# Kernel tuning notes

Hardware: AMD Instinct MI355X
Metric: run time of the kernel (lower is better)

Reference implementation:

```python
import jax, jax.numpy as jnp
import numpy as np

UNITS = 1024
EMBED = 512
K = 32000
HIDDEN_LAYERS = 2
BATCH = 64
SEQ = 256
ALPHA = 0.2  # leaky_relu slope


def _leaky_relu(z):
    return jnp.where(z > 0, z, ALPHA * z)


def setup_inputs() -> dict:
    key = jax.random.key(0)
    ks = jax.random.split(key, 10)
    s_in = 1.0 / np.sqrt(UNITS)
    s_e = 1.0 / np.sqrt(EMBED)
    return {
        "x": jax.random.randint(ks[0], (BATCH, SEQ), 0, K),
        "x_embedding": jax.random.normal(ks[1], (K, EMBED), dtype=jnp.float32) * 0.05,
        "w_y": jax.random.normal(ks[2], (UNITS, UNITS), dtype=jnp.float32) * s_in,
        "w_x": jax.random.normal(ks[3], (EMBED, UNITS), dtype=jnp.float32) * s_e,
        "b_in": jax.random.uniform(ks[4], (UNITS,), dtype=jnp.float32, minval=-0.05, maxval=0.05),
        "w_hidden": jax.random.normal(ks[5], (HIDDEN_LAYERS, UNITS, UNITS), dtype=jnp.float32) * s_in,
        "b_hidden": jax.random.uniform(ks[6], (HIDDEN_LAYERS, UNITS), dtype=jnp.float32, minval=-0.05, maxval=0.05),
        "w_out": jax.random.normal(ks[7], (UNITS, UNITS), dtype=jnp.float32) * s_in,
        "b_out": jax.random.uniform(ks[8], (UNITS,), dtype=jnp.float32, minval=-0.05, maxval=0.05),
        "h0": jax.random.uniform(ks[9], (1, UNITS), dtype=jnp.float32, minval=-0.05, maxval=0.05),
    }


def reference(x, x_embedding, w_y, w_x, b_in, w_hidden, b_hidden, w_out, b_out, h0):
    n = x.shape[0]
    # Gather all embeddings up front: [n, T, E] -> time-major [T, n, E]
    xe_all = jnp.swapaxes(x_embedding[x], 0, 1)

    def step(y0, xe):
        # MLPUnit: sum of input projections + bias, inner activation
        h = _leaky_relu(y0 @ w_y + xe @ w_x + b_in)

        def layer(hc, wb):
            w, bb = wb
            return _leaky_relu(hc @ w + bb), None

        h, _ = jax.lax.scan(layer, h, (w_hidden, b_hidden))
        y1 = y0 + (h @ w_out + b_out)  # highway residual
        return y1, y1

    y0 = jnp.broadcast_to(h0, (n, h0.shape[1]))
    _, yr = jax.lax.scan(step, y0, xe_all)  # [T, n, units]
    return jnp.swapaxes(yr, 0, 1)  # [n, T, units]
```

## Files before the change

### kernel.cpp

```cpp
#include <hip/hip_runtime.h>


constexpr int B = 64, T = 256, U = 1024, E = 512;
constexpr int BU = B * U;
constexpr int APITCH = 1156;
constexpr int RPITCH = 264;
constexpr int WOPITCH = 9;

#define LRELU(v) ((v) > 0.f ? (v) : 0.2f * (v))

using f4 = float __attribute__((ext_vector_type(4)));

__device__ __forceinline__ void llc_store(float* p, float v) {
  __hip_atomic_store(p, v, __ATOMIC_RELAXED, __HIP_MEMORY_SCOPE_AGENT);
}
__device__ __forceinline__ unsigned llc_flag(const unsigned* p) {
  return __hip_atomic_load(p, __ATOMIC_RELAXED, __HIP_MEMORY_SCOPE_AGENT);
}
__device__ __forceinline__ void llc_post(unsigned* p, unsigned v) {
  __hip_atomic_store(p, v, __ATOMIC_RELAXED, __HIP_MEMORY_SCOPE_AGENT);
}

#define COMPUTE_ACC(WB)                                          \
  do {                                                           \
    _Pragma("unroll") for (int r = 0; r < 8; ++r) acc[r] =       \
        (f4){0.f, 0.f, 0.f, 0.f};                                \
    _Pragma("unroll") for (int q = 0; q < 4; ++q) {              \
      const f4 w0 = WB[4 * q], w1 = WB[4 * q + 1];               \
      const f4 w2 = WB[4 * q + 2], w3 = WB[4 * q + 3];           \
      const int ab = abase_k + 4 * q;                            \
      _Pragma("unroll") for (int r = 0; r < 8; ++r) {            \
        f4 a = *(const f4*)&a_s[r * APITCH + ab];                \
        acc[r] += a.x * w0 + a.y * w1 + a.z * w2 + a.w * w3;     \
      }                                                          \
    }                                                            \
  } while (0)

__global__ void k_init(unsigned* __restrict__ flags) {
  int tid = blockIdx.x * 256 + threadIdx.x;
  if (tid < 512) flags[tid] = 0u;
}

__global__ __launch_bounds__(256) void k_xproj(
    const int* __restrict__ x, const float* __restrict__ emb,
    const float* __restrict__ w_x, const float* __restrict__ b_in,
    float* __restrict__ xp) {
  __shared__ float a_s[64][36];
  __shared__ float w_s[32][64];
  __shared__ int idxs[64];
  const int tid = threadIdx.x;
  const int m0 = blockIdx.x * 64;
  const int c0 = blockIdx.y * 64;
  if (tid < 64) {
    int m = m0 + tid;
    idxs[tid] = x[(m & 63) * T + (m >> 6)];
  }
  __syncthreads();
  const int rq = tid >> 4, cq = tid & 15;
  float acc[4][4] = {};
  for (int k0 = 0; k0 < E; k0 += 32) {
#pragma unroll
    for (int rep = 0; rep < 8; ++rep) {
      int e = rep * 256 + tid;
      int r = e >> 5, k = e & 31;
      a_s[r][k] = emb[(size_t)idxs[r] * E + k0 + k];
    }
#pragma unroll
    for (int rep = 0; rep < 2; ++rep) {
      int e = rep * 256 + tid;
      int kr = e >> 4, q = e & 15;
      *(float4*)&w_s[kr][4 * q] =
          *(const float4*)(w_x + (size_t)(k0 + kr) * U + c0 + 4 * q);
    }
    __syncthreads();
#pragma unroll
    for (int kc = 0; kc < 32; kc += 4) {
      float4 a4[4], w4[4];
#pragma unroll
      for (int i = 0; i < 4; ++i) a4[i] = *(const float4*)&a_s[4 * rq + i][kc];
#pragma unroll
      for (int kk = 0; kk < 4; ++kk)
        w4[kk] = *(const float4*)&w_s[kc + kk][4 * cq];
#pragma unroll
      for (int i = 0; i < 4; ++i) {
        const float av[4] = {a4[i].x, a4[i].y, a4[i].z, a4[i].w};
#pragma unroll
        for (int kk = 0; kk < 4; ++kk) {
          acc[i][0] += av[kk] * w4[kk].x;
          acc[i][1] += av[kk] * w4[kk].y;
          acc[i][2] += av[kk] * w4[kk].z;
          acc[i][3] += av[kk] * w4[kk].w;
        }
      }
    }
    __syncthreads();
  }
  const float4 bb = *(const float4*)(b_in + c0 + 4 * cq);
  const float bv[4] = {bb.x, bb.y, bb.z, bb.w};
#pragma unroll
  for (int i = 0; i < 4; ++i) {
    float4 o;
    o.x = acc[i][0] + bv[0];
    o.y = acc[i][1] + bv[1];
    o.z = acc[i][2] + bv[2];
    o.w = acc[i][3] + bv[3];
    *(float4*)(xp + (size_t)(m0 + 4 * rq + i) * U + c0 + 4 * cq) = o;
  }
}

__global__ __launch_bounds__(512, 2) void k_seq(
    const float* __restrict__ xp, const float* __restrict__ w_y,
    const float* __restrict__ w_h, const float* __restrict__ b_h,
    const float* __restrict__ w_out, const float* __restrict__ b_out,
    const float* __restrict__ h0, float* __restrict__ out,
    float* __restrict__ slots, unsigned* __restrict__ flags) {
  __shared__ float a_s[8 * APITCH];
  __shared__ float red2[64 * RPITCH];
  __shared__ float c2_s[32], u0_s[32];
  const int tid = threadIdx.x;
  const int bid = blockIdx.x;
  const int cg = ((bid & 7) << 2) | ((bid >> 3) & 3);
  const int rg = bid >> 5;
  const int w = tid >> 6, l = tid & 63;
  const int ci = l & 7;
  const int sp = w * 8 + (l >> 3);
  const int cb = 4 * ci, k0 = 16 * sp;
  const int abase_k = 36 * (sp >> 1) + 16 * (sp & 1);
  const int frow = 8 * rg + (tid >> 5);
  const int fu = 32 * cg + (tid & 31);
  const int tb = tid >> 8;
  const int kq = ((tid & 255) + 8 * cg) & 255;
  const int lofs = 36 * (kq >> 3) + ((4 * kq) & 31);

  float* const wos = red2;
  float* const wys = a_s;
  f4 w2reg[16];
#pragma unroll
  for (int jj = 0; jj < 16; ++jj) w2reg[jj] = (f4){0.f, 0.f, 0.f, 0.f};
  f4 c2a = (f4){0.f, 0.f, 0.f, 0.f}, u0a = (f4){0.f, 0.f, 0.f, 0.f};
  {
    f4 nx0, nx1, nx2, nx3, nwy;
    {
      const float* wo = w_out + (size_t)tid * U;
      nx0 = *(const f4*)wo;
      nx1 = *(const f4*)(wo + 4);
      const float* wo2 = w_out + (size_t)(tid + 512) * U;
      nx2 = *(const f4*)wo2;
      nx3 = *(const f4*)(wo2 + 4);
      if (tid < 64)
        nwy = *(const f4*)(w_y + (size_t)(tid >> 3) * U + 32 * cg +
                           4 * (tid & 7));
    }
    for (int mi = 0; mi < 128; ++mi) {
      const int m0 = mi * 8;
#pragma unroll
      for (int q = 0; q < 4; ++q) {
        wos[tid * WOPITCH + q] = nx0[q];
        wos[tid * WOPITCH + 4 + q] = nx1[q];
        wos[(tid + 512) * WOPITCH + q] = nx2[q];
        wos[(tid + 512) * WOPITCH + 4 + q] = nx3[q];
      }
      if (tid < 64) *(f4*)&wys[(tid >> 3) * 36 + 4 * (tid & 7)] = nwy;
      __syncthreads();
      if (mi < 127) {
        const int m1 = m0 + 8;
        const float* wo = w_out + (size_t)tid * U + m1;
        nx0 = *(const f4*)wo;
        nx1 = *(const f4*)(wo + 4);
        const float* wo2 = w_out + (size_t)(tid + 512) * U + m1;
        nx2 = *(const f4*)wo2;
        nx3 = *(const f4*)(wo2 + 4);
        if (tid < 64)
          nwy = *(const f4*)(w_y + (size_t)(m1 + (tid >> 3)) * U + 32 * cg +
                             4 * (tid & 7));
      }
#pragma unroll
      for (int mm = 0; mm < 8; ++mm) {
        const f4 wy = *(const f4*)&wys[mm * 36 + cb];
#pragma unroll
        for (int jj = 0; jj < 16; ++jj)
          w2reg[jj] += wos[(16 * sp + jj) * WOPITCH + mm] * wy;
        if (tid < 8) {
          c2a += b_out[m0 + mm] * wy;
          u0a += h0[m0 + mm] * wy;
        }
      }
      __syncthreads();
    }
  }
  if (tid < 8) {
    *(f4*)&c2_s[cb] = c2a;
    *(f4*)&u0_s[cb] = u0a;
  }
  __syncthreads();
  float u_reg = 0.f, y_reg = 0.f, c2_lane = 0.f;
  if (tid < 256) {
    c2_lane = c2_s[tid & 31];
    u_reg = u0_s[tid & 31];
    y_reg = h0[fu];
    float h1 = LRELU(u_reg + xp[(size_t)frow * U + fu]);
    llc_store(slots + (size_t)frow * U + fu, h1);
  }
  asm volatile("" ::: "memory");
  __builtin_amdgcn_s_waitcnt(0);
  __syncthreads();
  if (tid == 0) llc_post(&flags[rg * 32 + cg], 1u);

  f4 wreg[16];
  {
    const float* wp = w_h + (size_t)k0 * U + 32 * cg + cb;
#pragma unroll
    for (int jj = 0; jj < 16; ++jj) wreg[jj] = *(const f4*)(wp + (size_t)jj * U);
  }

  for (int Q = 1; Q <= 3 * T; ++Q) {
    const int j = (Q - 1) % 3, t = (Q - 1) / 3;
    const float* Asrc =
        slots + (size_t)((Q + 1) & 1) * BU + (size_t)(8 * rg) * U;
    float* slotw = slots + (size_t)(Q & 1) * BU;
    if (tid < 64) {
      const unsigned tgt = (unsigned)Q;
      const unsigned* fp = &flags[rg * 32 + (l & 31)];
      while (!__all(llc_flag(fp) >= tgt)) __builtin_amdgcn_s_sleep(1);
    }
    __syncthreads();
    asm volatile("" ::: "memory");
    float preA = 0.f, preB = 0.f;
    if (tid < 256) {
      if (j == 0)
        preA = b_h[fu];
      else if (j == 1)
        preA = b_h[U + fu];
      else {
        if (t < T - 1) preA = xp[((size_t)(t + 1) * B + frow) * U + fu];
        preB = b_out[fu];
      }
    }
    {
      const float* pb = Asrc + 4 * kq;
      f4 av0, av1, av2, av3;
      asm volatile("global_load_dwordx4 %0, %1, off sc1"
                   : "=v"(av0)
                   : "v"(pb + (size_t)tb * U));
      asm volatile("global_load_dwordx4 %0, %1, off sc1"
                   : "=v"(av1)
                   : "v"(pb + (size_t)(tb + 2) * U));
      asm volatile("global_load_dwordx4 %0, %1, off sc1"
                   : "=v"(av2)
                   : "v"(pb + (size_t)(tb + 4) * U));
      asm volatile("global_load_dwordx4 %0, %1, off sc1"
                   : "=v"(av3)
                   : "v"(pb + (size_t)(tb + 6) * U));
      asm volatile("s_waitcnt vmcnt(0)" ::: "memory");
      *(f4*)&a_s[(tb + 0) * APITCH + lofs] = av0;
      *(f4*)&a_s[(tb + 2) * APITCH + lofs] = av1;
      *(f4*)&a_s[(tb + 4) * APITCH + lofs] = av2;
      *(f4*)&a_s[(tb + 6) * APITCH + lofs] = av3;
    }
    __syncthreads();
    f4 acc[8];
    if (j == 2)
      COMPUTE_ACC(w2reg);
    else
      COMPUTE_ACC(wreg);
#pragma unroll
    for (int r = 0; r < 8; ++r)
      *(f4*)&red2[sp * RPITCH + r * 32 + cb] = acc[r];
    __syncthreads();
    if (tid < 256) {
      float s0 = 0.f, s1 = 0.f, s2 = 0.f, s3 = 0.f;
#pragma unroll
      for (int z = 0; z < 64; z += 4) {
        s0 += red2[(z + 0) * RPITCH + tid];
        s1 += red2[(z + 1) * RPITCH + tid];
        s2 += red2[(z + 2) * RPITCH + tid];
        s3 += red2[(z + 3) * RPITCH + tid];
      }
      const float sum = (s0 + s1) + (s2 + s3);
      const size_t yi = (size_t)frow * U + fu;
      if (j < 2) {
        llc_store(slotw + yi, LRELU(sum + preA));
      } else {
        u_reg += sum + c2_lane;
        llc_store(slotw + yi, LRELU(u_reg + preA));
      }
    }
    asm volatile("" ::: "memory");
    __builtin_amdgcn_s_waitcnt(0);
    __syncthreads();
    if (tid == 0) llc_post(&flags[rg * 32 + cg], (unsigned)(Q + 1));
    if (j == 2) {
      f4 acc2[8];
      {
        f4* acc = acc2;
        if (true) COMPUTE_ACC(wreg);
      }
#pragma unroll
      for (int r = 0; r < 8; ++r)
        *(f4*)&red2[sp * RPITCH + r * 32 + cb] = acc2[r];
      __syncthreads();
      if (tid < 256) {
        float s0 = 0.f, s1 = 0.f, s2 = 0.f, s3 = 0.f;
#pragma unroll
        for (int z = 0; z < 64; z += 4) {
          s0 += red2[(z + 0) * RPITCH + tid];
          s1 += red2[(z + 1) * RPITCH + tid];
          s2 += red2[(z + 2) * RPITCH + tid];
          s3 += red2[(z + 3) * RPITCH + tid];
        }
        y_reg += (s0 + s1) + (s2 + s3) + preB;
        out[((size_t)frow * T + t) * U + fu] = y_reg;
      }
    }
    if (Q < 3 * T) {
      const float* Wn = (j == 0) ? (w_h + (size_t)U * U)
                       : (j == 1) ? w_out
                                  : w_h;
      const float* wp = Wn + (size_t)k0 * U + 32 * cg + cb;
#pragma unroll
      for (int jj = 0; jj < 16; ++jj)
        wreg[jj] = *(const f4*)(wp + (size_t)jj * U);
    }
  }
}

extern "C" void kernel_launch(void* const* d_in, const int* in_sizes, int n_in,
                              void* d_out, int out_size, void* d_ws,
                              size_t ws_size, hipStream_t stream) {
  const int* x = (const int*)d_in[0];
  const float* emb = (const float*)d_in[1];
  const float* w_y = (const float*)d_in[2];
  const float* w_x = (const float*)d_in[3];
  const float* b_in = (const float*)d_in[4];
  const float* w_h = (const float*)d_in[5];
  const float* b_h = (const float*)d_in[6];
  const float* w_out = (const float*)d_in[7];
  const float* b_out = (const float*)d_in[8];
  const float* h0 = (const float*)d_in[9];
  float* out = (float*)d_out;

  float* ws = (float*)d_ws;
  float* xpb = ws;
  float* slots = xpb + (size_t)T * B * U;
  float* ybuf_dead = slots + 2 * (size_t)BU;
  unsigned* flags = (unsigned*)(ybuf_dead + (size_t)BU);

  k_init<<<2, 256, 0, stream>>>(flags);
  dim3 g1(256, 16);
  k_xproj<<<g1, 256, 0, stream>>>(x, emb, w_x, b_in, xpb);

  void* args[] = {&xpb,  &w_y,   &w_h, &b_h,   &w_out,
                  &b_out, &h0,   &out, &slots, &flags};
  hipLaunchCooperativeKernel((void*)k_seq, dim3(256), dim3(512), args, 0u,
                             stream);
}
```

Baseline: 4.836 ms.

## Split batch into two half-streams and pipeline them to overlap sync latency

Splits each block's 8-row batch slice into two 4-row halves (A and B), each with its own flag array, and interleaves them. While one half's global stores and inter-block flag wait are in flight, the other half's matmul runs, hiding cross-block sync latency. It also fuses the output projection for the highway residual into the same pass as the next-step w_y-composed projection (TILE4D), which removes the separate extra compute and reduction phase at j==2. The cost is more barriers and flag posts per step, plus doubled flag storage and a more intricate ordering that must stay deadlock-free.

```diff
diff --git a/kernel.cpp b/kernel.cpp
--- a/kernel.cpp
+++ b/kernel.cpp
@@ -21,19 +21,44 @@
   __hip_atomic_store(p, v, __ATOMIC_RELAXED, __HIP_MEMORY_SCOPE_AGENT);
 }
 
-#define COMPUTE_ACC(WB)                                          \
-  do {                                                           \
-    _Pragma("unroll") for (int r = 0; r < 8; ++r) acc[r] =       \
-        (f4){0.f, 0.f, 0.f, 0.f};                                \
-    _Pragma("unroll") for (int q = 0; q < 4; ++q) {              \
-      const f4 w0 = WB[4 * q], w1 = WB[4 * q + 1];               \
-      const f4 w2 = WB[4 * q + 2], w3 = WB[4 * q + 3];           \
-      const int ab = abase_k + 4 * q;                            \
-      _Pragma("unroll") for (int r = 0; r < 8; ++r) {            \
-        f4 a = *(const f4*)&a_s[r * APITCH + ab];                \
-        acc[r] += a.x * w0 + a.y * w1 + a.z * w2 + a.w * w3;     \
-      }                                                          \
-    }                                                            \
+#define TILE4(ACC, WB, AS)                                                \
+  do {                                                                    \
+    _Pragma("unroll") for (int q = 0; q < 4; ++q) {                       \
+      const f4 w0 = WB[4 * q], w1 = WB[4 * q + 1];                        \
+      const f4 w2v = WB[4 * q + 2], w3 = WB[4 * q + 3];                   \
+      const int ab = abase_k + 4 * q;                                     \
+      _Pragma("unroll") for (int r = 0; r < 4; ++r) {                     \
+        f4 a = *(const f4*)&AS[r * APITCH + ab];                          \
+        ACC[r] += a.x * w0 + a.y * w1 + a.z * w2v + a.w * w3;             \
+      }                                                                   \
+    }                                                                     \
+  } while (0)
+#define TILE4D(ACC, ACCY, WBM, WBY, AS)                                   \
+  do {                                                                    \
+    _Pragma("unroll") for (int q = 0; q < 4; ++q) {                       \
+      const f4 m0 = WBM[4 * q], m1 = WBM[4 * q + 1];                      \
+      const f4 m2 = WBM[4 * q + 2], m3 = WBM[4 * q + 3];                  \
+      const f4 y0 = WBY[4 * q], y1 = WBY[4 * q + 1];                      \
+      const f4 y2 = WBY[4 * q + 2], y3 = WBY[4 * q + 3];                  \
+      const int ab = abase_k + 4 * q;                                     \
+      _Pragma("unroll") for (int r = 0; r < 4; ++r) {                     \
+        f4 a = *(const f4*)&AS[r * APITCH + ab];                          \
+        ACC[r] += a.x * m0 + a.y * m1 + a.z * m2 + a.w * m3;              \
+        ACCY[r] += a.x * y0 + a.y * y1 + a.z * y2 + a.w * y3;             \
+      }                                                                   \
+    }                                                                     \
+  } while (0)
+#define RED64(SUM)                                                        \
+  float SUM;                                                              \
+  do {                                                                    \
+    float s0 = 0.f, s1 = 0.f, s2 = 0.f, s3 = 0.f;                         \
+    _Pragma("unroll") for (int z = 0; z < 64; z += 4) {                   \
+      s0 += red2[(z + 0) * RPITCH + tid];                                 \
+      s1 += red2[(z + 1) * RPITCH + tid];                                 \
+      s2 += red2[(z + 2) * RPITCH + tid];                                 \
+      s3 += red2[(z + 3) * RPITCH + tid];                                 \
+    }                                                                     \
+    SUM = (s0 + s1) + (s2 + s3);                                          \
   } while (0)
 
 __global__ void k_init(unsigned* __restrict__ flags) {
@@ -114,7 +139,8 @@
     const float* __restrict__ w_out, const float* __restrict__ b_out,
     const float* __restrict__ h0, float* __restrict__ out,
     float* __restrict__ slots, unsigned* __restrict__ flags) {
-  __shared__ float a_s[8 * APITCH];
+  __shared__ float a_sA[4 * APITCH];
+  __shared__ float a_sB[4 * APITCH];
   __shared__ float red2[64 * RPITCH];
   __shared__ float c2_s[32], u0_s[32];
   const int tid = threadIdx.x;
@@ -126,14 +152,18 @@
   const int sp = w * 8 + (l >> 3);
   const int cb = 4 * ci, k0 = 16 * sp;
   const int abase_k = 36 * (sp >> 1) + 16 * (sp & 1);
-  const int frow = 8 * rg + (tid >> 5);
+  const int ro = (tid & 127) >> 5;
   const int fu = 32 * cg + (tid & 31);
+  const int rowA = 4 * rg + ro;
+  const int rowB = 32 + rowA;
   const int tb = tid >> 8;
   const int kq = ((tid & 255) + 8 * cg) & 255;
   const int lofs = 36 * (kq >> 3) + ((4 * kq) & 31);
+  unsigned* const flagsA = flags;
+  unsigned* const flagsB = flags + 256;
 
   float* const wos = red2;
-  float* const wys = a_s;
+  float* const wys = a_sA;
   f4 w2reg[16];
 #pragma unroll
   for (int jj = 0; jj < 16; ++jj) w2reg[jj] = (f4){0.f, 0.f, 0.f, 0.f};
@@ -193,19 +223,44 @@
     *(f4*)&u0_s[cb] = u0a;
   }
   __syncthreads();
-  float u_reg = 0.f, y_reg = 0.f, c2_lane = 0.f;
-  if (tid < 256) {
+
+  float uA = 0.f, uB = 0.f, yA = 0.f, yB = 0.f, c2_lane = 0.f;
+  if (tid < 128) {
     c2_lane = c2_s[tid & 31];
-    u_reg = u0_s[tid & 31];
-    y_reg = h0[fu];
-    float h1 = LRELU(u_reg + xp[(size_t)frow * U + fu]);
-    llc_store(slots + (size_t)frow * U + fu, h1);
+    uA = u0_s[tid & 31];
+    uB = uA;
+    float h1A = LRELU(uA + xp[(size_t)rowA * U + fu]);
+    float h1B = LRELU(uB + xp[(size_t)rowB * U + fu]);
+    llc_store(slots + (size_t)rowA * U + fu, h1A);
+    llc_store(slots + (size_t)rowB * U + fu, h1B);
+  } else if (tid < 256) {
+    yA = h0[fu];
+    yB = yA;
   }
   asm volatile("" ::: "memory");
   __builtin_amdgcn_s_waitcnt(0);
   __syncthreads();
-  if (tid == 0) llc_post(&flags[rg * 32 + cg], 1u);
-
+  if (tid == 0) {
+    llc_post(&flagsA[rg * 32 + cg], 1u);
+    llc_post(&flagsB[rg * 32 + cg], 1u);
+  }
+  {
+    if (tid < 64) {
+      const unsigned* fp = &flagsA[rg * 32 + (l & 31)];
+      while (!__all(llc_flag(fp) >= 1u)) __builtin_amdgcn_s_sleep(1);
+    }
+    __syncthreads();
+    asm volatile("" ::: "memory");
+    const float* pb = slots + (size_t)(4 * rg) * U + 4 * kq;
+    f4 av0, av1;
+    asm volatile("global_load_dwordx4 %0, %1, off sc1"
+                 : "=v"(av0) : "v"(pb + (size_t)tb * U));
+    asm volatile("global_load_dwordx4 %0, %1, off sc1"
+                 : "=v"(av1) : "v"(pb + (size_t)(tb + 2) * U));
+    asm volatile("s_waitcnt vmcnt(0)" ::: "memory");
+    *(f4*)&a_sA[(tb + 0) * APITCH + lofs] = av0;
+    *(f4*)&a_sA[(tb + 2) * APITCH + lofs] = av1;
+  }
   f4 wreg[16];
   {
     const float* wp = w_h + (size_t)k0 * U + 32 * cg + cb;
@@ -213,109 +268,130 @@
     for (int jj = 0; jj < 16; ++jj) wreg[jj] = *(const f4*)(wp + (size_t)jj * U);
   }
 
-  for (int Q = 1; Q <= 3 * T; ++Q) {
-    const int j = (Q - 1) % 3, t = (Q - 1) / 3;
-    const float* Asrc =
-        slots + (size_t)((Q + 1) & 1) * BU + (size_t)(8 * rg) * U;
-    float* slotw = slots + (size_t)(Q & 1) * BU;
+  for (int S = 1; S <= 3 * T; ++S) {
+    const int j = (S - 1) % 3, t = (S - 1) / 3;
+    float* const slotw = slots + (size_t)(S & 1) * BU;
     if (tid < 64) {
-      const unsigned tgt = (unsigned)Q;
-      const unsigned* fp = &flags[rg * 32 + (l & 31)];
+      const unsigned tgt = (unsigned)S;
+      const unsigned* fp = &flagsB[rg * 32 + (l & 31)];
       while (!__all(llc_flag(fp) >= tgt)) __builtin_amdgcn_s_sleep(1);
     }
     __syncthreads();
     asm volatile("" ::: "memory");
-    float preA = 0.f, preB = 0.f;
-    if (tid < 256) {
-      if (j == 0)
-        preA = b_h[fu];
-      else if (j == 1)
-        preA = b_h[U + fu];
-      else {
-        if (t < T - 1) preA = xp[((size_t)(t + 1) * B + frow) * U + fu];
-        preB = b_out[fu];
-      }
-    }
+    f4 bv0, bv1;
     {
-      const float* pb = Asrc + 4 * kq;
-      f4 av0, av1, av2, av3;
+      const float* pb =
+          slots + (size_t)((S + 1) & 1) * BU + (size_t)(32 + 4 * rg) * U + 4 * kq;
       asm volatile("global_load_dwordx4 %0, %1, off sc1"
-                   : "=v"(av0)
-                   : "v"(pb + (size_t)tb * U));
+                   : "=v"(bv0) : "v"(pb + (size_t)tb * U));
       asm volatile("global_load_dwordx4 %0, %1, off sc1"
-                   : "=v"(av1)
-                   : "v"(pb + (size_t)(tb + 2) * U));
-      asm volatile("global_load_dwordx4 %0, %1, off sc1"
-                   : "=v"(av2)
-                   : "v"(pb + (size_t)(tb + 4) * U));
-      asm volatile("global_load_dwordx4 %0, %1, off sc1"
-                   : "=v"(av3)
-                   : "v"(pb + (size_t)(tb + 6) * U));
-      asm volatile("s_waitcnt vmcnt(0)" ::: "memory");
-      *(f4*)&a_s[(tb + 0) * APITCH + lofs] = av0;
-      *(f4*)&a_s[(tb + 2) * APITCH + lofs] = av1;
-      *(f4*)&a_s[(tb + 4) * APITCH + lofs] = av2;
-      *(f4*)&a_s[(tb + 6) * APITCH + lofs] = av3;
-    }
-    __syncthreads();
-    f4 acc[8];
+                   : "=v"(bv1) : "v"(pb + (size_t)(tb + 2) * U));
+    }
+    float preU = 0.f, preXA = 0.f, preXB = 0.f, preY = 0.f;
+    if (tid < 128) {
+      if (j < 2)
+        preU = b_h[j * U + fu];
+      else if (t < T - 1) {
+        preXA = xp[((size_t)(t + 1) * B + rowA) * U + fu];
+        preXB = xp[((size_t)(t + 1) * B + rowB) * U + fu];
+      }
+    } else if (tid < 256 && j == 2)
+      preY = b_out[fu];
+    f4 acc[4], accY[4];
+#pragma unroll
+    for (int r = 0; r < 4; ++r) acc[r] = accY[r] = (f4){0.f, 0.f, 0.f, 0.f};
     if (j == 2)
-      COMPUTE_ACC(w2reg);
+      TILE4D(acc, accY, w2reg, wreg, a_sA);
     else
-      COMPUTE_ACC(wreg);
-#pragma unroll
-    for (int r = 0; r < 8; ++r)
+      TILE4(acc, wreg, a_sA);
+#pragma unroll
+    for (int r = 0; r < 4; ++r)
       *(f4*)&red2[sp * RPITCH + r * 32 + cb] = acc[r];
-    __syncthreads();
-    if (tid < 256) {
-      float s0 = 0.f, s1 = 0.f, s2 = 0.f, s3 = 0.f;
-#pragma unroll
-      for (int z = 0; z < 64; z += 4) {
-        s0 += red2[(z + 0) * RPITCH + tid];
-        s1 += red2[(z + 1) * RPITCH + tid];
-        s2 += red2[(z + 2) * RPITCH + tid];
-        s3 += red2[(z + 3) * RPITCH + tid];
-      }
-      const float sum = (s0 + s1) + (s2 + s3);
-      const size_t yi = (size_t)frow * U + fu;
+    if (j == 2) {
+#pragma unroll
+      for (int r = 0; r < 4; ++r)
+        *(f4*)&red2[sp * RPITCH + 128 + r * 32 + cb] = accY[r];
+    }
+    __syncthreads();
+    if (tid < 128) {
+      RED64(sum);
+      float* dst = slotw + (size_t)rowA * U + fu;
       if (j < 2) {
-        llc_store(slotw + yi, LRELU(sum + preA));
+        llc_store(dst, LRELU(sum + preU));
       } else {
-        u_reg += sum + c2_lane;
-        llc_store(slotw + yi, LRELU(u_reg + preA));
-      }
+        uA += sum + c2_lane;
+        llc_store(dst, LRELU(uA + preXA));
+      }
+    } else if (tid < 256 && j == 2) {
+      RED64(sum);
+      yA += sum + preY;
     }
     asm volatile("" ::: "memory");
     __builtin_amdgcn_s_waitcnt(0);
     __syncthreads();
-    if (tid == 0) llc_post(&flags[rg * 32 + cg], (unsigned)(Q + 1));
+    if (tid == 0) llc_post(&flagsA[rg * 32 + cg], (unsigned)(S + 1));
+    if (j == 2 && tid >= 128 && tid < 256)
+      out[((size_t)rowA * T + t) * U + fu] = yA;
+    *(f4*)&a_sB[(tb + 0) * APITCH + lofs] = bv0;
+    *(f4*)&a_sB[(tb + 2) * APITCH + lofs] = bv1;
+    if (tid < 64) {
+      const unsigned tgt = (unsigned)(S + 1);
+      const unsigned* fp = &flagsA[rg * 32 + (l & 31)];
+      while (!__all(llc_flag(fp) >= tgt)) __builtin_amdgcn_s_sleep(1);
+    }
+    __syncthreads();
+    asm volatile("" ::: "memory");
+    f4 av0, av1;
+    if (S < 3 * T) {
+      const float* pb =
+          slots + (size_t)(S & 1) * BU + (size_t)(4 * rg) * U + 4 * kq;
+      asm volatile("global_load_dwordx4 %0, %1, off sc1"
+                   : "=v"(av0) : "v"(pb + (size_t)tb * U));
+      asm volatile("global_load_dwordx4 %0, %1, off sc1"
+                   : "=v"(av1) : "v"(pb + (size_t)(tb + 2) * U));
+    }
+#pragma unroll
+    for (int r = 0; r < 4; ++r) acc[r] = accY[r] = (f4){0.f, 0.f, 0.f, 0.f};
+    if (j == 2)
+      TILE4D(acc, accY, w2reg, wreg, a_sB);
+    else
+      TILE4(acc, wreg, a_sB);
+#pragma unroll
+    for (int r = 0; r < 4; ++r)
+      *(f4*)&red2[sp * RPITCH + r * 32 + cb] = acc[r];
     if (j == 2) {
-      f4 acc2[8];
-      {
-        f4* acc = acc2;
-        if (true) COMPUTE_ACC(wreg);
-      }
-#pragma unroll
-      for (int r = 0; r < 8; ++r)
-        *(f4*)&red2[sp * RPITCH + r * 32 + cb] = acc2[r];
-      __syncthreads();
-      if (tid < 256) {
-        float s0 = 0.f, s1 = 0.f, s2 = 0.f, s3 = 0.f;
-#pragma unroll
-        for (int z = 0; z < 64; z += 4) {
-          s0 += red2[(z + 0) * RPITCH + tid];
-          s1 += red2[(z + 1) * RPITCH + tid];
-          s2 += red2[(z + 2) * RPITCH + tid];
-          s3 += red2[(z + 3) * RPITCH + tid];
-        }
-        y_reg += (s0 + s1) + (s2 + s3) + preB;
-        out[((size_t)frow * T + t) * U + fu] = y_reg;
-      }
-    }
-    if (Q < 3 * T) {
+#pragma unroll
+      for (int r = 0; r < 4; ++r)
+        *(f4*)&red2[sp * RPITCH + 128 + r * 32 + cb] = accY[r];
+    }
+    __syncthreads();
+    if (tid < 128) {
+      RED64(sum);
+      float* dst = slotw + (size_t)rowB * U + fu;
+      if (j < 2) {
+        llc_store(dst, LRELU(sum + preU));
+      } else {
+        uB += sum + c2_lane;
+        llc_store(dst, LRELU(uB + preXB));
+      }
+    } else if (tid < 256 && j == 2) {
+      RED64(sum);
+      yB += sum + preY;
+    }
+    asm volatile("" ::: "memory");
+    __builtin_amdgcn_s_waitcnt(0);
+    __syncthreads();
+    if (tid == 0) llc_post(&flagsB[rg * 32 + cg], (unsigned)(S + 1));
+    if (j == 2 && tid >= 128 && tid < 256)
+      out[((size_t)rowB * T + t) * U + fu] = yB;
+    if (S < 3 * T) {
+      *(f4*)&a_sA[(tb + 0) * APITCH + lofs] = av0;
+      *(f4*)&a_sA[(tb + 2) * APITCH + lofs] = av1;
+    }
+    if (S < 3 * T) {
       const float* Wn = (j == 0) ? (w_h + (size_t)U * U)
-                       : (j == 1) ? w_out
-                                  : w_h;
+                        : (j == 1) ? w_out
+                                   : w_h;
       const float* wp = Wn + (size_t)k0 * U + 32 * cg + cb;
 #pragma unroll
       for (int jj = 0; jj < 16; ++jj)
@@ -342,15 +418,15 @@
   float* ws = (float*)d_ws;
   float* xpb = ws;
   float* slots = xpb + (size_t)T * B * U;
-  float* ybuf_dead = slots + 2 * (size_t)BU;
-  unsigned* flags = (unsigned*)(ybuf_dead + (size_t)BU);
+  float* dead = slots + 2 * (size_t)BU;
+  unsigned* flags = (unsigned*)(dead + (size_t)BU);
 
   k_init<<<2, 256, 0, stream>>>(flags);
   dim3 g1(256, 16);
   k_xproj<<<g1, 256, 0, stream>>>(x, emb, w_x, b_in, xpb);
 
-  void* args[] = {&xpb,  &w_y,   &w_h, &b_h,   &w_out,
-                  &b_out, &h0,   &out, &slots, &flags};
+  void* args[] = {&xpb,   &w_y, &w_h, &b_h,   &w_out,
+                  &b_out, &h0,  &out, &slots, &flags};
   hipLaunchCooperativeKernel((void*)k_seq, dim3(256), dim3(512), args, 0u,
                              stream);
 }
```

Measured after the change: 6.447 ms. 33.3% more time.

## Replace global per-step barrier with per-slab flag waits before each activation load

Applied to the files above, without the earlier changes.

Each step used to start with one wavefront spinning on all 32 producer flags for its row group, followed by a block-wide barrier, before any activation data was loaded. Now every wavefront waits only on the flag of the column slab it is about to load and issues that load immediately, in a rotated order per wavefront and block. The aim is to overlap waiting with loading and drop one __syncthreads per step. The cost is more flag polling traffic, since every wavefront polls four flags, plus a changed LDS staging pattern.

```diff
diff --git a/kernel.cpp b/kernel.cpp
--- a/kernel.cpp
+++ b/kernel.cpp
@@ -128,9 +128,7 @@
   const int abase_k = 36 * (sp >> 1) + 16 * (sp & 1);
   const int frow = 8 * rg + (tid >> 5);
   const int fu = 32 * cg + (tid & 31);
-  const int tb = tid >> 8;
-  const int kq = ((tid & 255) + 8 * cg) & 255;
-  const int lofs = 36 * (kq >> 3) + ((4 * kq) & 31);
+  const int srow = l >> 3, scol = l & 7;
 
   float* const wos = red2;
   float* const wys = a_s;
@@ -210,7 +208,8 @@
   {
     const float* wp = w_h + (size_t)k0 * U + 32 * cg + cb;
 #pragma unroll
-    for (int jj = 0; jj < 16; ++jj) wreg[jj] = *(const f4*)(wp + (size_t)jj * U);
+    for (int jj = 0; jj < 16; ++jj)
+      wreg[jj] = *(const f4*)(wp + (size_t)jj * U);
   }
 
   for (int Q = 1; Q <= 3 * T; ++Q) {
@@ -218,13 +217,6 @@
     const float* Asrc =
         slots + (size_t)((Q + 1) & 1) * BU + (size_t)(8 * rg) * U;
     float* slotw = slots + (size_t)(Q & 1) * BU;
-    if (tid < 64) {
-      const unsigned tgt = (unsigned)Q;
-      const unsigned* fp = &flags[rg * 32 + (l & 31)];
-      while (!__all(llc_flag(fp) >= tgt)) __builtin_amdgcn_s_sleep(1);
-    }
-    __syncthreads();
-    asm volatile("" ::: "memory");
     float preA = 0.f, preB = 0.f;
     if (tid < 256) {
       if (j == 0)
@@ -237,25 +229,32 @@
       }
     }
     {
-      const float* pb = Asrc + 4 * kq;
-      f4 av0, av1, av2, av3;
-      asm volatile("global_load_dwordx4 %0, %1, off sc1"
-                   : "=v"(av0)
-                   : "v"(pb + (size_t)tb * U));
-      asm volatile("global_load_dwordx4 %0, %1, off sc1"
-                   : "=v"(av1)
-                   : "v"(pb + (size_t)(tb + 2) * U));
-      asm volatile("global_load_dwordx4 %0, %1, off sc1"
-                   : "=v"(av2)
-                   : "v"(pb + (size_t)(tb + 4) * U));
-      asm volatile("global_load_dwordx4 %0, %1, off sc1"
-                   : "=v"(av3)
-                   : "v"(pb + (size_t)(tb + 6) * U));
+      f4 sv0, sv1, sv2, sv3;
+      int sd0, sd1, sd2, sd3;
+#define STAGE_SLAB(I, SV, SD)                                              \
+      {                                                                    \
+        const int pc = ((w << 2) + I + cg) & 31;                           \
+        const unsigned* fp = &flags[rg * 32 + pc];                         \
+        while (!__all(llc_flag(fp) >= (unsigned)Q))                        \
+          __builtin_amdgcn_s_sleep(1);                                     \
+        asm volatile("" ::: "memory");                                     \
+        const float* pb =                                                  \
+            Asrc + (size_t)srow * U + (size_t)(32 * pc + 4 * scol);        \
+        asm volatile("global_load_dwordx4 %0, %1, off sc1"                 \
+                     : "=v"(SV)                                            \
+                     : "v"(pb));                                           \
+        SD = srow * APITCH + 36 * pc + 4 * scol;                           \
+      }
+      STAGE_SLAB(0, sv0, sd0)
+      STAGE_SLAB(1, sv1, sd1)
+      STAGE_SLAB(2, sv2, sd2)
+      STAGE_SLAB(3, sv3, sd3)
+#undef STAGE_SLAB
       asm volatile("s_waitcnt vmcnt(0)" ::: "memory");
-      *(f4*)&a_s[(tb + 0) * APITCH + lofs] = av0;
-      *(f4*)&a_s[(tb + 2) * APITCH + lofs] = av1;
-      *(f4*)&a_s[(tb + 4) * APITCH + lofs] = av2;
-      *(f4*)&a_s[(tb + 6) * APITCH + lofs] = av3;
+      *(f4*)&a_s[sd0] = sv0;
+      *(f4*)&a_s[sd1] = sv1;
+      *(f4*)&a_s[sd2] = sv2;
+      *(f4*)&a_s[sd3] = sv3;
     }
     __syncthreads();
     f4 acc[8];
@@ -313,9 +312,9 @@
       }
     }
     if (Q < 3 * T) {
-      const float* Wn = (j == 0) ? (w_h + (size_t)U * U)
-                       : (j == 1) ? w_out
-                                  : w_h;
+      const float* Wn = (j == 0)   ? (w_h + (size_t)U * U)
+                        : (j == 1) ? w_out
+                                   : w_h;
       const float* wp = Wn + (size_t)k0 * U + 32 * cg + cb;
 #pragma unroll
       for (int jj = 0; jj < 16; ++jj)
@@ -342,15 +341,15 @@
   float* ws = (float*)d_ws;
   float* xpb = ws;
   float* slots = xpb + (size_t)T * B * U;
-  float* ybuf_dead = slots + 2 * (size_t)BU;
-  unsigned* flags = (unsigned*)(ybuf_dead + (size_t)BU);
+  float* dead = slots + 2 * (size_t)BU;
+  unsigned* flags = (unsigned*)(dead + (size_t)BU);
 
   k_init<<<2, 256, 0, stream>>>(flags);
   dim3 g1(256, 16);
   k_xproj<<<g1, 256, 0, stream>>>(x, emb, w_x, b_in, xpb);
 
-  void* args[] = {&xpb,  &w_y,   &w_h, &b_h,   &w_out,
-                  &b_out, &h0,   &out, &slots, &flags};
+  void* args[] = {&xpb,   &w_y, &w_h, &b_h,   &w_out,
+                  &b_out, &h0,  &out, &slots, &flags};
   hipLaunchCooperativeKernel((void*)k_seq, dim3(256), dim3(512), args, 0u,
                              stream);
 }
```

Result: slower. 5.237 ms (+8.3%).
